# Performance work log

Measured on AMD Instinct MI355X. Metric: run time of the kernel, lower is better.

Reference implementation:

```python
import jax, jax.numpy as jnp
import numpy as np

N_NODES = 50000
N_EDGES = 1250000
IN_CH = 64
HID = 64
N_CLASSES = 10
N_GRAPHS = 128


def _xavier(key, shape):
    fan_out, fan_in = shape
    limit = np.sqrt(6.0 / (fan_in + fan_out))
    return jax.random.uniform(key, shape, jnp.float32, -limit, limit)


def setup_inputs() -> dict:
    key = jax.random.key(0)
    ks = jax.random.split(key, 12)
    x = jax.random.normal(ks[0], (N_NODES, IN_CH), jnp.float32)
    edge_index = jax.random.randint(ks[1], (2, N_EDGES), 0, N_NODES, jnp.int64)
    batch = jnp.sort(jax.random.randint(ks[2], (N_NODES,), 0, N_GRAPHS, jnp.int64))
    return {
        "x": x,
        "edge_index": edge_index,
        "batch": batch,
        # GraphConv i: lin_rel (weight+bias) applied to aggregated neighbors,
        # lin_root (no bias) applied to self features. Weights are [out, in].
        "W1_rel": _xavier(ks[3], (HID, IN_CH)), "b1": jnp.zeros((HID,), jnp.float32),
        "W1_root": _xavier(ks[4], (HID, IN_CH)),
        "W2_rel": _xavier(ks[5], (HID, HID)), "b2": jnp.zeros((HID,), jnp.float32),
        "W2_root": _xavier(ks[6], (HID, HID)),
        "W3_rel": _xavier(ks[7], (HID, HID)), "b3": jnp.zeros((HID,), jnp.float32),
        "W3_root": _xavier(ks[8], (HID, HID)),
        "W_lin": _xavier(ks[9], (N_CLASSES, HID)), "b_lin": jnp.zeros((N_CLASSES,), jnp.float32),
    }


def _graph_conv(x, src, dst, W_rel, b, W_root):
    # sum-aggregate neighbor features: gather at src, scatter-add at dst
    agg = jax.ops.segment_sum(x[src], dst, num_segments=N_NODES)  # [N, F]
    return agg @ W_rel.T + b + x @ W_root.T


def reference(x, edge_index, batch, W1_rel, b1, W1_root, W2_rel, b2, W2_root,
              W3_rel, b3, W3_root, W_lin, b_lin):
    src, dst = edge_index[0], edge_index[1]
    h = jax.nn.relu(_graph_conv(x, src, dst, W1_rel, b1, W1_root))
    h = jax.nn.relu(_graph_conv(h, src, dst, W2_rel, b2, W2_root))
    h = _graph_conv(h, src, dst, W3_rel, b3, W3_root)
    # global mean pool over graphs
    sums = jax.ops.segment_sum(h, batch, num_segments=N_GRAPHS)        # [G, HID]
    counts = jax.ops.segment_sum(jnp.ones((h.shape[0],), h.dtype), batch,
                                 num_segments=N_GRAPHS)
    pooled = sums / jnp.maximum(counts, 1.0)[:, None]
    out = pooled @ W_lin.T + b_lin  # dropout inactive in eval mode
    return (pooled, out)
```

## Files before the change

### kernel.cpp

```cpp
#include <hip/hip_runtime.h>

#define N_NODES   50000
#define HID       64
#define N_GRAPHS  128
#define N_CLASSES 10
#define NP        196
#define EPA       8192
#define PCAP      8192

typedef __attribute__((ext_vector_type(8))) short short8;
typedef __attribute__((ext_vector_type(4))) float f32x4;

__device__ __forceinline__ unsigned bf16rne(float f) {
    unsigned u = __float_as_uint(f);
    return (u + 0x7fffu + ((u >> 16) & 1u)) >> 16;
}
__device__ __forceinline__ unsigned pack_bf16x2(float lo, float hi) {
    return bf16rne(lo) | (bf16rne(hi) << 16);
}



__global__ void cvt_kernel(const float* __restrict__ x, unsigned short* __restrict__ xb,
                           int* __restrict__ gcursor, const int* __restrict__ batch,
                           int* __restrict__ gstart) {
    int i = blockIdx.x * blockDim.x + threadIdx.x;
    if (blockIdx.x == 0 && threadIdx.x < NP) gcursor[threadIdx.x] = 0;
    if (i < N_NODES) {
        int b = batch[i];
        int bp = (i > 0) ? batch[i - 1] : -1;
        for (int g = bp + 1; g <= b; ++g) gstart[g] = i;
        if (i == N_NODES - 1)
            for (int g = b + 1; g <= N_GRAPHS; ++g) gstart[g] = N_NODES;
    }
    if (i < N_NODES * 16) {
        float4 v = ((const float4*)x)[i];
        uint2 o;
        o.x = pack_bf16x2(v.x, v.y);
        o.y = pack_bf16x2(v.z, v.w);
        ((uint2*)xb)[i] = o;
    }
}


__global__ __launch_bounds__(256) void bucket_kernel(
    const int* __restrict__ src, const int* __restrict__ dst,
    int* __restrict__ gcursor, unsigned* __restrict__ packed, int E) {
    __shared__ int hist[NP], scp[NP], base[NP], cnt2[NP];
    __shared__ int sc[256];
    __shared__ unsigned stag[EPA];
    const int t = threadIdx.x;
    const int e0 = blockIdx.x * EPA;
    const int e1 = min(e0 + EPA, E);
    for (int i = t; i < NP; i += 256) { hist[i] = 0; cnt2[i] = 0; }
    __syncthreads();
    for (int e = e0 + t; e < e1; e += 256)
        atomicAdd(&hist[dst[e] >> 8], 1);
    __syncthreads();
    sc[t] = (t < NP) ? hist[t] : 0;
    __syncthreads();
    for (int off = 1; off < 256; off <<= 1) {
        int add = (t >= off) ? sc[t - off] : 0;
        __syncthreads();
        sc[t] += add;
        __syncthreads();
    }
    if (t < NP) {
        scp[t] = sc[t] - hist[t];
        if (hist[t] > 0) base[t] = atomicAdd(&gcursor[t], hist[t]);
    }
    __syncthreads();
    for (int e = e0 + t; e < e1; e += 256) {
        int d = dst[e], s = src[e];
        int p = d >> 8;
        int idx = scp[p] + atomicAdd(&cnt2[p], 1);
        stag[idx] = (unsigned)s | ((unsigned)(d & 255) << 16) | ((unsigned)p << 24);
    }
    __syncthreads();
    const int n = e1 - e0;
    for (int i = t; i < n; i += 256) {
        unsigned v = stag[i];
        int p = v >> 24;
        packed[(size_t)p * PCAP + base[p] + (i - scp[p])] = v & 0x00FFFFFFu;
    }
}

__global__ __launch_bounds__(256) void build_kernel(
    const unsigned* __restrict__ packed, const int* __restrict__ gcursor,
    int* __restrict__ offsets, unsigned short* __restrict__ csr,
    int* __restrict__ sums_zero) {
    __shared__ int hist[256], lofs[256], cnt[256], sc[256], gv[256];
    __shared__ unsigned short lcsr[PCAP];
    const int p = blockIdx.x, t = threadIdx.x;

    if (p == 0) {
        for (int i = t; i < N_GRAPHS * 64; i += 256) sums_zero[i] = 0;
    }

    int v = (t < NP) ? gcursor[t] : 0;
    sc[t] = v; gv[t] = v;
    __syncthreads();
    for (int off = 1; off < 256; off <<= 1) {
        int add = (t >= off) ? sc[t - off] : 0;
        __syncthreads();
        sc[t] += add;
        __syncthreads();
    }
    const int pb = sc[p] - gv[p];
    const int ne = gv[p];
    if (p == NP - 1 && t == 0) offsets[N_NODES] = sc[NP - 1];
    __syncthreads();

    const unsigned* mypk = packed + (size_t)p * PCAP;
    hist[t] = 0; cnt[t] = 0;
    __syncthreads();
    for (int i = t; i < ne; i += 256)
        atomicAdd(&hist[(mypk[i] >> 16) & 255], 1);
    __syncthreads();
    sc[t] = hist[t];
    __syncthreads();
    for (int off = 1; off < 256; off <<= 1) {
        int add = (t >= off) ? sc[t - off] : 0;
        __syncthreads();
        sc[t] += add;
        __syncthreads();
    }
    lofs[t] = sc[t] - hist[t];
    int node = p * 256 + t;
    if (node < N_NODES) offsets[node] = pb + lofs[t];
    __syncthreads();
    for (int i = t; i < ne; i += 256) {
        unsigned vv = mypk[i];
        int dl = (vv >> 16) & 255;
        int slot = lofs[dl] + atomicAdd(&cnt[dl], 1);
        lcsr[slot] = (unsigned short)(vv & 0xFFFFu);
    }
    __syncthreads();
    for (int i = t; i < ne; i += 256) csr[pb + i] = lcsr[i];
}


template <int RELU, int POOL>
__global__ __launch_bounds__(256) void layer_kernel(
    const unsigned short* __restrict__ hin,
    const int* __restrict__ offsets, const unsigned short* __restrict__ csr_src,
    const float* __restrict__ Wrel, const float* __restrict__ bias,
    const float* __restrict__ Wroot, unsigned short* __restrict__ hout,
    const int* __restrict__ batch, float* __restrict__ sums) {
    __shared__ short8 wfrag[2][4][2][4][16];
    __shared__ unsigned short agg_lds[32][72];

    const int tid = threadIdx.x;
    const int w = tid >> 6, lane = tid & 63;
    const int g0 = blockIdx.x * 32;

    for (int f = tid; f < 1024; f += 256) {
        int m = f >> 9;
        int r = f & 511;
        int t = r >> 7, s = (r >> 6) & 1, q = (r >> 4) & 3, c = r & 15;
        const float* W = m ? Wroot : Wrel;
        const float4* pw = (const float4*)(W + (t * 16 + c) * 64 + s * 32 + q * 8);
        float4 v0 = pw[0], v1 = pw[1];
        short8 fr;
        fr[0] = (short)bf16rne(v0.x); fr[1] = (short)bf16rne(v0.y);
        fr[2] = (short)bf16rne(v0.z); fr[3] = (short)bf16rne(v0.w);
        fr[4] = (short)bf16rne(v1.x); fr[5] = (short)bf16rne(v1.y);
        fr[6] = (short)bf16rne(v1.z); fr[7] = (short)bf16rne(v1.w);
        wfrag[m][t][s][q][c] = fr;
    }

    {
        const int rg = lane >> 3;
        const int cg = lane & 7;
        const int nb = g0 + w * 8;
        int myoff = (lane < 9) ? offsets[min(nb + lane, N_NODES)] : 0;
        for (int i = 0; i < 8; ++i) {
            const int beg = __shfl(myoff, i), end = __shfl(myoff, i + 1);
            float acc[8] = {0.f, 0.f, 0.f, 0.f, 0.f, 0.f, 0.f, 0.f};
            for (int base = beg; base < end; base += 64) {
                int cnt = min(64, end - base);
                int sidx = (base + lane < end) ? (int)csr_src[base + lane] : 0;
                for (int kb = 0; kb < cnt; kb += 32) {
                    uint4 u[4];
#pragma unroll
                    for (int p = 0; p < 4; ++p) {
                        int e = kb + 8 * p + rg;
                        int r = __shfl(sidx, e);
                        u[p] = (e < cnt) ? *((const uint4*)(hin + (size_t)r * 64) + cg)
                                         : make_uint4(0u, 0u, 0u, 0u);
                    }
#pragma unroll
                    for (int p = 0; p < 4; ++p) {
                        acc[0] += __uint_as_float(u[p].x << 16);
                        acc[1] += __uint_as_float(u[p].x & 0xffff0000u);
                        acc[2] += __uint_as_float(u[p].y << 16);
                        acc[3] += __uint_as_float(u[p].y & 0xffff0000u);
                        acc[4] += __uint_as_float(u[p].z << 16);
                        acc[5] += __uint_as_float(u[p].z & 0xffff0000u);
                        acc[6] += __uint_as_float(u[p].w << 16);
                        acc[7] += __uint_as_float(u[p].w & 0xffff0000u);
                    }
                }
            }
#pragma unroll
            for (int m = 8; m <= 32; m <<= 1)
#pragma unroll
                for (int j = 0; j < 8; ++j)
                    acc[j] += __shfl_xor(acc[j], m);
            if (rg == 0) {
                uint4 o;
                o.x = pack_bf16x2(acc[0], acc[1]);
                o.y = pack_bf16x2(acc[2], acc[3]);
                o.z = pack_bf16x2(acc[4], acc[5]);
                o.w = pack_bf16x2(acc[6], acc[7]);
                *((uint4*)&agg_lds[w * 8 + i][cg * 8]) = o;
            }
        }
    }

    __syncthreads();

    const int ng = w >> 1;
    const int th = w & 1;
    const int q = lane >> 4, c = lane & 15;
    const int n0 = g0 + ng * 16;

    short8 a_agg[2], a_x[2];
#pragma unroll
    for (int s = 0; s < 2; ++s) {
        a_agg[s] = *(const short8*)&agg_lds[ng * 16 + c][s * 32 + q * 8];
        a_x[s]   = *(const short8*)(hin + (size_t)min(n0 + c, N_NODES - 1) * 64 + s * 32 + q * 8);
    }

    f32x4 acc4[2];
#pragma unroll
    for (int tt = 0; tt < 2; ++tt) {
        const int t = th * 2 + tt;
        float bv = bias[t * 16 + c];
        f32x4 a0 = {bv, bv, bv, bv};
        a0 = __builtin_amdgcn_mfma_f32_16x16x32_bf16(a_agg[0], wfrag[0][t][0][q][c], a0, 0, 0, 0);
        a0 = __builtin_amdgcn_mfma_f32_16x16x32_bf16(a_agg[1], wfrag[0][t][1][q][c], a0, 0, 0, 0);
        a0 = __builtin_amdgcn_mfma_f32_16x16x32_bf16(a_x[0],   wfrag[1][t][0][q][c], a0, 0, 0, 0);
        a0 = __builtin_amdgcn_mfma_f32_16x16x32_bf16(a_x[1],   wfrag[1][t][1][q][c], a0, 0, 0, 0);
        acc4[tt] = a0;
    }

    if (POOL) {
        int nlast = n0 + 15;
        int b0 = batch[min(n0, N_NODES - 1)];
        int b15 = (nlast < N_NODES) ? batch[nlast] : -1;
        if (b0 == b15) {
#pragma unroll
            for (int tt = 0; tt < 2; ++tt) {
                const int t = th * 2 + tt;
                float s = acc4[tt][0] + acc4[tt][1] + acc4[tt][2] + acc4[tt][3];
                s += __shfl_xor(s, 16);
                s += __shfl_xor(s, 32);
                if (q == 0) atomicAdd(&sums[b0 * 64 + t * 16 + c], s);
            }
        } else {
#pragma unroll
            for (int r = 0; r < 4; ++r) {
                int n = n0 + q * 4 + r;
                if (n < N_NODES) {
                    int bq = batch[n];
#pragma unroll
                    for (int tt = 0; tt < 2; ++tt)
                        atomicAdd(&sums[bq * 64 + (th * 2 + tt) * 16 + c], acc4[tt][r]);
                }
            }
        }
    } else {
        __syncthreads();
#pragma unroll
        for (int tt = 0; tt < 2; ++tt) {
            const int t = th * 2 + tt;
#pragma unroll
            for (int r = 0; r < 4; ++r) {
                float v = acc4[tt][r];
                if (RELU) v = fmaxf(v, 0.f);
                agg_lds[ng * 16 + q * 4 + r][t * 16 + c] = (unsigned short)bf16rne(v);
            }
        }
        __syncthreads();
        {
            int row = w * 8 + (lane >> 3);
            int ch = (lane & 7) * 8;
            int n = g0 + row;
            if (n < N_NODES) {
                short8 v = *(const short8*)&agg_lds[row][ch];
                *(short8*)(hout + (size_t)n * 64 + ch) = v;
            }
        }
    }
}


__global__ void final_kernel(const float* __restrict__ sums, const int* __restrict__ gstart,
                             const float* __restrict__ Wlin, const float* __restrict__ blin,
                             float* __restrict__ out) {
    __shared__ float pl[64];
    int g = blockIdx.x, lane = threadIdx.x;
    float cdiv = fmaxf((float)(gstart[g + 1] - gstart[g]), 1.0f);
    float p = sums[g * 64 + lane] / cdiv;
    out[g * 64 + lane] = p;
    pl[lane] = p;
    __syncthreads();
    if (lane < N_CLASSES) {
        float o = blin[lane];
#pragma unroll
        for (int k = 0; k < 64; ++k) o += pl[k] * Wlin[lane * 64 + k];
        out[N_GRAPHS * 64 + g * N_CLASSES + lane] = o;
    }
}


extern "C" void kernel_launch(void* const* d_in, const int* in_sizes, int n_in,
                              void* d_out, int out_size, void* d_ws, size_t ws_size,
                              hipStream_t stream) {
    const float* x     = (const float*)d_in[0];
    const int*   ei    = (const int*)d_in[1];
    const int*   batch = (const int*)d_in[2];
    const float* W1r = (const float*)d_in[3];
    const float* b1  = (const float*)d_in[4];
    const float* W1o = (const float*)d_in[5];
    const float* W2r = (const float*)d_in[6];
    const float* b2  = (const float*)d_in[7];
    const float* W2o = (const float*)d_in[8];
    const float* W3r = (const float*)d_in[9];
    const float* b3  = (const float*)d_in[10];
    const float* W3o = (const float*)d_in[11];
    const float* Wl  = (const float*)d_in[12];
    const float* bl  = (const float*)d_in[13];
    float* out = (float*)d_out;

    const int E = in_sizes[1] / 2;
    const int* src = ei;
    const int* dst = ei + E;

    char* p = (char*)d_ws;
    unsigned short* xb  = (unsigned short*)p; p += (size_t)N_NODES * 64 * 2;
    unsigned short* h1  = (unsigned short*)p; p += (size_t)N_NODES * 64 * 2;
    unsigned short* h2  = (unsigned short*)p; p += (size_t)N_NODES * 64 * 2;
    unsigned* packed    = (unsigned*)p; p += (size_t)NP * PCAP * 4;
    unsigned short* csr = (unsigned short*)p; p += (size_t)E * 2;
    int* offsets   = (int*)p;   p += (size_t)(N_NODES + 1) * 4;
    int* gcursor   = (int*)p;   p += NP * 4;
    float* sums    = (float*)p; p += (size_t)N_GRAPHS * 64 * 4;
    int* gstart    = (int*)p;   p += (N_GRAPHS + 1) * 4;

    const int NCHUNK = (E + EPA - 1) / EPA;
    cvt_kernel<<<(N_NODES * 16 + 255) / 256, 256, 0, stream>>>(x, xb, gcursor, batch, gstart);
    bucket_kernel<<<NCHUNK, 256, 0, stream>>>(src, dst, gcursor, packed, E);
    build_kernel<<<NP, 256, 0, stream>>>(packed, gcursor, offsets, csr, (int*)sums);

    const int LB = (N_NODES + 31) / 32;
    layer_kernel<1, 0><<<LB, 256, 0, stream>>>(xb, offsets, csr, W1r, b1, W1o, h1, batch, sums);
    layer_kernel<1, 0><<<LB, 256, 0, stream>>>(h1, offsets, csr, W2r, b2, W2o, h2, batch, sums);
    layer_kernel<0, 1><<<LB, 256, 0, stream>>>(h2, offsets, csr, W3r, b3, W3o, h1, batch, sums);

    final_kernel<<<N_GRAPHS, 64, 0, stream>>>(sums, gstart, Wl, bl, out);
}
```

Before: 234.2 us.

## Merge prep kernels and fold final pooling into last layer via completion counter

```diff
diff --git a/kernel.cpp b/kernel.cpp
--- a/kernel.cpp
+++ b/kernel.cpp
@@ -7,6 +7,9 @@
 #define NP        196
 #define EPA       8192
 #define PCAP      8192
+#define NCVT      3125
+#define LB3       1563
+#define FINAL_BLKS 8
 
 typedef __attribute__((ext_vector_type(8))) short short8;
 typedef __attribute__((ext_vector_type(4))) float f32x4;
@@ -21,81 +24,86 @@
 
 
 
-__global__ void cvt_kernel(const float* __restrict__ x, unsigned short* __restrict__ xb,
-                           int* __restrict__ gcursor, const int* __restrict__ batch,
-                           int* __restrict__ gstart) {
-    int i = blockIdx.x * blockDim.x + threadIdx.x;
-    if (blockIdx.x == 0 && threadIdx.x < NP) gcursor[threadIdx.x] = 0;
-    if (i < N_NODES) {
-        int b = batch[i];
-        int bp = (i > 0) ? batch[i - 1] : -1;
-        for (int g = bp + 1; g <= b; ++g) gstart[g] = i;
-        if (i == N_NODES - 1)
-            for (int g = b + 1; g <= N_GRAPHS; ++g) gstart[g] = N_NODES;
-    }
-    if (i < N_NODES * 16) {
+__global__ void init_kernel(int* __restrict__ gcursor, float* __restrict__ sums,
+                            int* __restrict__ done_ctr) {
+    int i = blockIdx.x * 256 + threadIdx.x;
+    if (i < NP) gcursor[i] = 0;
+    if (i < N_GRAPHS * 64) sums[i] = 0.f;
+    if (i == 0) *done_ctr = 0;
+}
+
+
+__global__ __launch_bounds__(256) void prep_kernel(
+    const float* __restrict__ x, const int* __restrict__ src,
+    const int* __restrict__ dst, const int* __restrict__ batch,
+    unsigned short* __restrict__ xb, int* __restrict__ gcursor,
+    unsigned* __restrict__ packed, int* __restrict__ gstart,
+    int E, int nchunk) {
+    __shared__ int hist[NP], scp[NP], base[NP], cnt2[NP];
+    __shared__ int sc[256];
+    __shared__ unsigned stag[EPA];
+    const int t = threadIdx.x;
+    const int vb = blockIdx.x;
+
+    if (vb < nchunk) {
+        const int e0 = vb * EPA;
+        const int e1 = min(e0 + EPA, E);
+        for (int i = t; i < NP; i += 256) { hist[i] = 0; cnt2[i] = 0; }
+        __syncthreads();
+        for (int e = e0 + t; e < e1; e += 256)
+            atomicAdd(&hist[dst[e] >> 8], 1);
+        __syncthreads();
+        sc[t] = (t < NP) ? hist[t] : 0;
+        __syncthreads();
+        for (int off = 1; off < 256; off <<= 1) {
+            int add = (t >= off) ? sc[t - off] : 0;
+            __syncthreads();
+            sc[t] += add;
+            __syncthreads();
+        }
+        if (t < NP) {
+            scp[t] = sc[t] - hist[t];
+            if (hist[t] > 0) base[t] = atomicAdd(&gcursor[t], hist[t]);
+        }
+        __syncthreads();
+        for (int e = e0 + t; e < e1; e += 256) {
+            int d = dst[e], s = src[e];
+            int p = d >> 8;
+            int idx = scp[p] + atomicAdd(&cnt2[p], 1);
+            stag[idx] = (unsigned)s | ((unsigned)(d & 255) << 16) | ((unsigned)p << 24);
+        }
+        __syncthreads();
+        const int n = e1 - e0;
+        for (int i = t; i < n; i += 256) {
+            unsigned v = stag[i];
+            int p = v >> 24;
+            packed[(size_t)p * PCAP + base[p] + (i - scp[p])] = v & 0x00FFFFFFu;
+        }
+    } else if (vb < nchunk + NCVT) {
+        int i = (vb - nchunk) * 256 + t;
         float4 v = ((const float4*)x)[i];
         uint2 o;
         o.x = pack_bf16x2(v.x, v.y);
         o.y = pack_bf16x2(v.z, v.w);
         ((uint2*)xb)[i] = o;
-    }
-}
-
-
-__global__ __launch_bounds__(256) void bucket_kernel(
-    const int* __restrict__ src, const int* __restrict__ dst,
-    int* __restrict__ gcursor, unsigned* __restrict__ packed, int E) {
-    __shared__ int hist[NP], scp[NP], base[NP], cnt2[NP];
-    __shared__ int sc[256];
-    __shared__ unsigned stag[EPA];
-    const int t = threadIdx.x;
-    const int e0 = blockIdx.x * EPA;
-    const int e1 = min(e0 + EPA, E);
-    for (int i = t; i < NP; i += 256) { hist[i] = 0; cnt2[i] = 0; }
-    __syncthreads();
-    for (int e = e0 + t; e < e1; e += 256)
-        atomicAdd(&hist[dst[e] >> 8], 1);
-    __syncthreads();
-    sc[t] = (t < NP) ? hist[t] : 0;
-    __syncthreads();
-    for (int off = 1; off < 256; off <<= 1) {
-        int add = (t >= off) ? sc[t - off] : 0;
-        __syncthreads();
-        sc[t] += add;
-        __syncthreads();
-    }
-    if (t < NP) {
-        scp[t] = sc[t] - hist[t];
-        if (hist[t] > 0) base[t] = atomicAdd(&gcursor[t], hist[t]);
-    }
-    __syncthreads();
-    for (int e = e0 + t; e < e1; e += 256) {
-        int d = dst[e], s = src[e];
-        int p = d >> 8;
-        int idx = scp[p] + atomicAdd(&cnt2[p], 1);
-        stag[idx] = (unsigned)s | ((unsigned)(d & 255) << 16) | ((unsigned)p << 24);
-    }
-    __syncthreads();
-    const int n = e1 - e0;
-    for (int i = t; i < n; i += 256) {
-        unsigned v = stag[i];
-        int p = v >> 24;
-        packed[(size_t)p * PCAP + base[p] + (i - scp[p])] = v & 0x00FFFFFFu;
+    } else {
+        int node = (vb - nchunk - NCVT) * 256 + t;
+        if (node < N_NODES) {
+            int b = batch[node];
+            int bp = (node > 0) ? batch[node - 1] : -1;
+            for (int g = bp + 1; g <= b; ++g) gstart[g] = node;
+            if (node == N_NODES - 1)
+                for (int g = b + 1; g <= N_GRAPHS; ++g) gstart[g] = N_NODES;
+        }
     }
 }
 
 __global__ __launch_bounds__(256) void build_kernel(
     const unsigned* __restrict__ packed, const int* __restrict__ gcursor,
-    int* __restrict__ offsets, unsigned short* __restrict__ csr,
-    int* __restrict__ sums_zero) {
+    int* __restrict__ offsets, unsigned short* __restrict__ csr) {
     __shared__ int hist[256], lofs[256], cnt[256], sc[256], gv[256];
     __shared__ unsigned short lcsr[PCAP];
     const int p = blockIdx.x, t = threadIdx.x;
-
-    if (p == 0) {
-        for (int i = t; i < N_GRAPHS * 64; i += 256) sums_zero[i] = 0;
-    }
 
     int v = (t < NP) ? gcursor[t] : 0;
     sc[t] = v; gv[t] = v;
@@ -146,7 +154,10 @@
     const int* __restrict__ offsets, const unsigned short* __restrict__ csr_src,
     const float* __restrict__ Wrel, const float* __restrict__ bias,
     const float* __restrict__ Wroot, unsigned short* __restrict__ hout,
-    const int* __restrict__ batch, float* __restrict__ sums) {
+    const int* __restrict__ batch, float* __restrict__ sums,
+    const int* __restrict__ gstart, const float* __restrict__ Wlin,
+    const float* __restrict__ blin, float* __restrict__ out,
+    int* __restrict__ done_ctr) {
     __shared__ short8 wfrag[2][4][2][4][16];
     __shared__ unsigned short agg_lds[32][72];
 
@@ -270,6 +281,35 @@
                 }
             }
         }
+
+        __threadfence();
+        __syncthreads();
+        __shared__ int s_old;
+        if (tid == 0) s_old = atomicAdd(done_ctr, 1);
+        __syncthreads();
+        if (s_old >= LB3 - FINAL_BLKS) {
+            if (tid == 0)
+                while (__hip_atomic_load(done_ctr, __ATOMIC_ACQUIRE,
+                                         __HIP_MEMORY_SCOPE_AGENT) < LB3) {}
+            __syncthreads();
+            const int slice = s_old - (LB3 - FINAL_BLKS);
+            for (int gi = 0; gi < 4; ++gi) {
+                int g = slice * 16 + w * 4 + gi;
+                float pv = __hip_atomic_load(&sums[g * 64 + lane],
+                               __ATOMIC_RELAXED, __HIP_MEMORY_SCOPE_AGENT);
+                float cdiv = fmaxf((float)(gstart[g + 1] - gstart[g]), 1.0f);
+                pv /= cdiv;
+                out[g * 64 + lane] = pv;
+                float o = (lane < N_CLASSES) ? blin[lane] : 0.f;
+#pragma unroll
+                for (int k = 0; k < 64; ++k) {
+                    float pk = __shfl(pv, k);
+                    if (lane < N_CLASSES) o += pk * Wlin[lane * 64 + k];
+                }
+                if (lane < N_CLASSES)
+                    out[N_GRAPHS * 64 + g * N_CLASSES + lane] = o;
+            }
+        }
     } else {
         __syncthreads();
 #pragma unroll
@@ -292,25 +332,6 @@
                 *(short8*)(hout + (size_t)n * 64 + ch) = v;
             }
         }
-    }
-}
-
-
-__global__ void final_kernel(const float* __restrict__ sums, const int* __restrict__ gstart,
-                             const float* __restrict__ Wlin, const float* __restrict__ blin,
-                             float* __restrict__ out) {
-    __shared__ float pl[64];
-    int g = blockIdx.x, lane = threadIdx.x;
-    float cdiv = fmaxf((float)(gstart[g + 1] - gstart[g]), 1.0f);
-    float p = sums[g * 64 + lane] / cdiv;
-    out[g * 64 + lane] = p;
-    pl[lane] = p;
-    __syncthreads();
-    if (lane < N_CLASSES) {
-        float o = blin[lane];
-#pragma unroll
-        for (int k = 0; k < 64; ++k) o += pl[k] * Wlin[lane * 64 + k];
-        out[N_GRAPHS * 64 + g * N_CLASSES + lane] = o;
     }
 }
 
@@ -348,16 +369,18 @@
     int* gcursor   = (int*)p;   p += NP * 4;
     float* sums    = (float*)p; p += (size_t)N_GRAPHS * 64 * 4;
     int* gstart    = (int*)p;   p += (N_GRAPHS + 1) * 4;
+    int* done_ctr  = (int*)p;   p += 4;
 
     const int NCHUNK = (E + EPA - 1) / EPA;
-    cvt_kernel<<<(N_NODES * 16 + 255) / 256, 256, 0, stream>>>(x, xb, gcursor, batch, gstart);
-    bucket_kernel<<<NCHUNK, 256, 0, stream>>>(src, dst, gcursor, packed, E);
-    build_kernel<<<NP, 256, 0, stream>>>(packed, gcursor, offsets, csr, (int*)sums);
-
-    const int LB = (N_NODES + 31) / 32;
-    layer_kernel<1, 0><<<LB, 256, 0, stream>>>(xb, offsets, csr, W1r, b1, W1o, h1, batch, sums);
-    layer_kernel<1, 0><<<LB, 256, 0, stream>>>(h1, offsets, csr, W2r, b2, W2o, h2, batch, sums);
-    layer_kernel<0, 1><<<LB, 256, 0, stream>>>(h2, offsets, csr, W3r, b3, W3o, h1, batch, sums);
-
-    final_kernel<<<N_GRAPHS, 64, 0, stream>>>(sums, gstart, Wl, bl, out);
-}
+    init_kernel<<<32, 256, 0, stream>>>(gcursor, sums, done_ctr);
+    prep_kernel<<<NCHUNK + NCVT + NP, 256, 0, stream>>>(
+        x, src, dst, batch, xb, gcursor, packed, gstart, E, NCHUNK);
+    build_kernel<<<NP, 256, 0, stream>>>(packed, gcursor, offsets, csr);
+
+    layer_kernel<1, 0><<<LB3, 256, 0, stream>>>(xb, offsets, csr, W1r, b1, W1o, h1,
+        batch, sums, gstart, Wl, bl, out, done_ctr);
+    layer_kernel<1, 0><<<LB3, 256, 0, stream>>>(h1, offsets, csr, W2r, b2, W2o, h2,
+        batch, sums, gstart, Wl, bl, out, done_ctr);
+    layer_kernel<0, 1><<<LB3, 256, 0, stream>>>(h2, offsets, csr, W3r, b3, W3o, h1,
+        batch, sums, gstart, Wl, bl, out, done_ctr);
+}
```

New measurement: 383.1 us. 63.5% more time.
